# Kernel tuning notes

Measured on AMD Instinct MI355X. Metric: run time of the kernel, lower is better.

Reference implementation:

```python
import jax, jax.numpy as jnp
import numpy as np

SEQ, B, XD = 2048, 4, 16
D, NH, DFF, L, M = 256, 8, 512, 2, 1024
DH = D // NH
NEG_INF = -1e9  # finite stand-in for -inf (same softmax result, grad-safe)


def setup_inputs() -> dict:
    key = jax.random.key(0)
    ks = iter(jax.random.split(key, 40))

    def w(shape, s=0.02):
        return jax.random.normal(next(ks), shape, dtype=jnp.float32) * s

    return {
        "x": jax.random.normal(next(ks), (SEQ, B, XD), dtype=jnp.float32),
        "y": jax.random.normal(next(ks), (SEQ, B), dtype=jnp.float32),
        "single_eval_pos": M,
        "xenc_w": w((D, XD)), "xenc_b": w((D,)),
        "yenc_w": w((D, 1)), "yenc_b": w((D,)),
        "in_proj_w": w((L, 3 * D, D)), "in_proj_b": w((L, 3 * D)),
        "out_proj_w": w((L, D, D)), "out_proj_b": w((L, D)),
        "ln1_g": jnp.ones((L, D), jnp.float32), "ln1_b": jnp.zeros((L, D), jnp.float32),
        "lin1_w": w((L, DFF, D)), "lin1_b": w((L, DFF)),
        "lin2_w": w((L, D, DFF)), "lin2_b": w((L, D)),
        "ln2_g": jnp.ones((L, D), jnp.float32), "ln2_b": jnp.zeros((L, D), jnp.float32),
        "head_w1": w((DFF, D)), "head_b1": w((DFF,)),
        "head_w2": w((1, DFF)), "head_b2": w((1,)),
    }


def _layer_norm(x, g, b, eps=1e-5):
    mu = jnp.mean(x, axis=-1, keepdims=True)
    var = jnp.var(x, axis=-1, keepdims=True)
    return (x - mu) * jax.lax.rsqrt(var + eps) * g + b


def _forward(x, y, M_, p):
    seq, batch = y.shape
    x_src = x @ p["xenc_w"].T + p["xenc_b"]                     # [seq, b, D]
    y_src = y[..., None] @ p["yenc_w"].T + p["yenc_b"]           # [seq, b, D]
    tokens = jnp.concatenate([x_src[:M_] + y_src[:M_], x_src[M_:]], axis=0)

    # prefix-block + diagonal mask: keep (j < M) or (i == j)
    i = jnp.arange(seq)
    keep = (i[None, :] < M_) | (i[:, None] == i[None, :])
    mask = jnp.where(keep, 0.0, NEG_INF).astype(tokens.dtype)    # [seq, seq]

    h = tokens
    for l in range(p["in_proj_w"].shape[0]):
        qkv = h @ p["in_proj_w"][l].T + p["in_proj_b"][l]        # [seq, b, 3D]
        q, k, v = jnp.split(qkv, 3, axis=-1)
        to_heads = lambda t: t.reshape(seq, batch, NH, DH).transpose(1, 2, 0, 3)
        q, k, v = to_heads(q), to_heads(k), to_heads(v)          # [b, h, s, dh]
        scores = jnp.einsum("bhqd,bhkd->bhqk", q, k) / np.float32(np.sqrt(DH)) + mask
        attn = jax.nn.softmax(scores, axis=-1)
        o = jnp.einsum("bhqk,bhkd->bhqd", attn, v)
        o = o.transpose(2, 0, 1, 3).reshape(seq, batch, D)
        o = o @ p["out_proj_w"][l].T + p["out_proj_b"][l]
        h = _layer_norm(h + o, p["ln1_g"][l], p["ln1_b"][l])      # post-norm
        ff = jax.nn.gelu(h @ p["lin1_w"][l].T + p["lin1_b"][l], approximate=False)
        ff = ff @ p["lin2_w"][l].T + p["lin2_b"][l]
        h = _layer_norm(h + ff, p["ln2_g"][l], p["ln2_b"][l])

    q_out = h[M_:]                                               # [seq-M, b, D]
    hid = jax.nn.gelu(q_out @ p["head_w1"].T + p["head_b1"], approximate=False)
    return hid @ p["head_w2"].T + p["head_b2"]                   # [seq-M, b, 1]


def reference(x, y, single_eval_pos, xenc_w, xenc_b, yenc_w, yenc_b,
              in_proj_w, in_proj_b, out_proj_w, out_proj_b,
              ln1_g, ln1_b, lin1_w, lin1_b, lin2_w, lin2_b, ln2_g, ln2_b,
              head_w1, head_b1, head_w2, head_b2):
    p = dict(xenc_w=xenc_w, xenc_b=xenc_b, yenc_w=yenc_w, yenc_b=yenc_b,
             in_proj_w=in_proj_w, in_proj_b=in_proj_b,
             out_proj_w=out_proj_w, out_proj_b=out_proj_b,
             ln1_g=ln1_g, ln1_b=ln1_b, lin1_w=lin1_w, lin1_b=lin1_b,
             lin2_w=lin2_w, lin2_b=lin2_b, ln2_g=ln2_g, ln2_b=ln2_b,
             head_w1=head_w1, head_b1=head_b1, head_w2=head_w2, head_b2=head_b2)
    return _forward(x, y, int(single_eval_pos), p)
```

## Files before the change

### kernel.cpp

```cpp
#include <hip/hip_runtime.h>
#include <hip/hip_bf16.h>
#include <math.h>

#define SEQ    2048
#define BATCH  4
#define XDIM   16
#define DMODEL 256
#define NHEAD  8
#define DH     32
#define DFF    512
#define NLAYER 2
#define MPOS   1024
#define ROWS   (SEQ*BATCH)

#define ATT_SCALE 0.17677669529663687f
#define BK 32

typedef __attribute__((ext_vector_type(8))) short bf16x8;
typedef __attribute__((ext_vector_type(4))) float f32x4;

__device__ __forceinline__ float gelu_exact(float x) {
    return 0.5f * x * (1.0f + erff(x * 0.70710678118654752f));
}
__device__ __forceinline__ short f2bf(float f) {
    unsigned int u = __float_as_uint(f);
    u += 0x7FFFu + ((u >> 16) & 1u);
    return (short)(u >> 16);
}
__device__ __forceinline__ float bf2f(unsigned short u) {
    return __uint_as_float(((unsigned int)u) << 16);
}
__device__ __forceinline__ void gload16(const unsigned short* g, unsigned short* l) {
    __builtin_amdgcn_global_load_lds(
        (const __attribute__((address_space(1))) unsigned int*)g,
        (__attribute__((address_space(3))) unsigned int*)l, 16, 0, 0);
}
#define VMWAIT(N) asm volatile("s_waitcnt vmcnt(" #N ")" ::: "memory")
__device__ __forceinline__ void pipe_barrier() {
    __builtin_amdgcn_sched_barrier(0);
    __builtin_amdgcn_s_barrier();
    __builtin_amdgcn_sched_barrier(0);
}

__global__ __launch_bounds__(256) void encode_cast(
    const float* __restrict__ x, const float* __restrict__ y,
    const float* __restrict__ xw, const float* __restrict__ xb,
    const float* __restrict__ yw, const float* __restrict__ yb,
    float* __restrict__ h, unsigned short* __restrict__ hb,
    const float* __restrict__ s0, const float* __restrict__ s1,
    const float* __restrict__ s2, const float* __restrict__ s3,
    const float* __restrict__ s4,
    unsigned short* __restrict__ d0, unsigned short* __restrict__ d1,
    unsigned short* __restrict__ d2, unsigned short* __restrict__ d3,
    unsigned short* __restrict__ d4)
{
    if (blockIdx.x < ROWS) {
        int row = blockIdx.x;
        int d   = threadIdx.x;
        int s   = row / BATCH;
        __shared__ float xs[XDIM];
        __shared__ float ys;
        if (d < XDIM) xs[d] = x[(size_t)row*XDIM + d];
        if (d == 0)   ys    = y[row];
        __syncthreads();
        float acc = xb[d];
        #pragma unroll
        for (int k = 0; k < XDIM; ++k) acc = fmaf(xs[k], xw[d*XDIM + k], acc);
        if (s < MPOS) acc += ys * yw[d] + yb[d];
        h[(size_t)row*DMODEL + d]  = acc;
        hb[(size_t)row*DMODEL + d] = (unsigned short)f2bf(acc);
        return;
    }
    int i = (blockIdx.x - ROWS)*256 + threadIdx.x;
    if (i >= 147456) return;
    const float* s; unsigned short* d; int off;
    if      (i <  49152) { s = s0; d = d0; off = i; }
    else if (i <  65536) { s = s1; d = d1; off = i - 49152; }
    else if (i <  98304) { s = s2; d = d2; off = i - 65536; }
    else if (i < 131072) { s = s3; d = d3; off = i - 98304; }
    else                 { s = s4; d = d4; off = i - 131072; }
    float4 a = *(const float4*)(s + (size_t)off*8);
    float4 c = *(const float4*)(s + (size_t)off*8 + 4);
    ushort4 u0, u1;
    u0.x=(unsigned short)f2bf(a.x); u0.y=(unsigned short)f2bf(a.y);
    u0.z=(unsigned short)f2bf(a.z); u0.w=(unsigned short)f2bf(a.w);
    u1.x=(unsigned short)f2bf(c.x); u1.y=(unsigned short)f2bf(c.y);
    u1.z=(unsigned short)f2bf(c.z); u1.w=(unsigned short)f2bf(c.w);
    *(ushort4*)(d + (size_t)off*8)     = u0;
    *(ushort4*)(d + (size_t)off*8 + 4) = u1;
}

__global__ __launch_bounds__(256) void gemm_qkv(
    const unsigned short* __restrict__ A, const unsigned short* __restrict__ B,
    const float* __restrict__ bias,
    unsigned short* __restrict__ Qg, unsigned short* __restrict__ Kg,
    unsigned short* __restrict__ Vg, int K)
{
    __shared__ unsigned short As[3][128][BK];
    __shared__ unsigned short Bs[3][64][BK];
    int tid  = threadIdx.x;
    int w    = tid >> 6, lane = tid & 63;
    int col  = lane & 15, quad = lane >> 4;
    int m0   = blockIdx.y * 128, n0 = blockIdx.x * 64;
    int l4   = lane >> 2, c8 = (lane & 3) * 8;

    f32x4 acc[2][4];
    #pragma unroll
    for (int i = 0; i < 2; ++i)
        #pragma unroll
        for (int j = 0; j < 4; ++j) acc[i][j] = (f32x4){0.f,0.f,0.f,0.f};

    const unsigned short* ga = A + (size_t)(m0 + w*32 + l4)*K + c8;
    const unsigned short* gb = B + (size_t)(n0 + w*16 + l4)*K + c8;

    const int NS = K / BK;
    gload16(ga,                  &As[0][w*32     ][0]);
    gload16(ga + (size_t)16*K,   &As[0][w*32 + 16][0]);
    gload16(gb,                  &Bs[0][w*16     ][0]);
    gload16(ga + BK,                  &As[1][w*32     ][0]);
    gload16(ga + BK + (size_t)16*K,   &As[1][w*32 + 16][0]);
    gload16(gb + BK,                  &Bs[1][w*16     ][0]);

    int bcur = 0;
    for (int s = 0; s < NS; ++s) {
        if (s == NS - 1) { VMWAIT(0); } else { VMWAIT(3); }
        pipe_barrier();
        if (s + 2 < NS) {
            int bpre = bcur + 2; if (bpre >= 3) bpre -= 3;
            int k2 = (s + 2) * BK;
            gload16(ga + k2,                &As[bpre][w*32     ][0]);
            gload16(ga + k2 + (size_t)16*K, &As[bpre][w*32 + 16][0]);
            gload16(gb + k2,                &Bs[bpre][w*16     ][0]);
        }
        bf16x8 af[2], bfr[4];
        #pragma unroll
        for (int i = 0; i < 2; ++i) af[i]  = *(const bf16x8*)&As[bcur][w*32 + i*16 + col][quad*8];
        #pragma unroll
        for (int j = 0; j < 4; ++j) bfr[j] = *(const bf16x8*)&Bs[bcur][j*16 + col][quad*8];
        #pragma unroll
        for (int i = 0; i < 2; ++i)
            #pragma unroll
            for (int j = 0; j < 4; ++j)
                acc[i][j] = __builtin_amdgcn_mfma_f32_16x16x32_bf16(bfr[j], af[i], acc[i][j], 0, 0, 0);
        bcur = (bcur == 2) ? 0 : bcur + 1;
    }

    int region = n0 >> 8;
    if (region < 2) {
        #pragma unroll
        for (int i = 0; i < 2; ++i) {
            int m = m0 + w*32 + i*16 + col;
            int s = m >> 2, bidx = m & 3;
            #pragma unroll
            for (int j = 0; j < 4; ++j) {
                int ng = n0 + j*16 + quad*4;
                float4 bi = *(const float4*)&bias[ng];
                ushort4 u;
                u.x=(unsigned short)f2bf(acc[i][j][0] + bi.x);
                u.y=(unsigned short)f2bf(acc[i][j][1] + bi.y);
                u.z=(unsigned short)f2bf(acc[i][j][2] + bi.z);
                u.w=(unsigned short)f2bf(acc[i][j][3] + bi.w);
                int np = ng - (region << 8);
                int hh = np >> 5, d = np & 31;
                int bh = bidx*NHEAD + hh;
                if (region == 0)
                    *(ushort4*)(Qg + ((size_t)(bh*SEQ + s))*DH + d) = u;
                else
                    *(ushort4*)(Kg + ((size_t)(bh*SEQ + s))*DH + d) = u;
            }
        }
    } else {
        __syncthreads();
        unsigned short* T3 = (unsigned short*)As;
        #pragma unroll
        for (int i = 0; i < 2; ++i) {
            int mi = w*32 + i*16 + col;
            int ss = mi >> 2, bidx = mi & 3;
            #pragma unroll
            for (int j = 0; j < 4; ++j) {
                int ni = j*16 + quad*4;
                float4 bi = *(const float4*)&bias[n0 + ni];
                T3[((ni    )*4 + bidx)*32 + ss] = (unsigned short)f2bf(acc[i][j][0] + bi.x);
                T3[((ni + 1)*4 + bidx)*32 + ss] = (unsigned short)f2bf(acc[i][j][1] + bi.y);
                T3[((ni + 2)*4 + bidx)*32 + ss] = (unsigned short)f2bf(acc[i][j][2] + bi.z);
                T3[((ni + 3)*4 + bidx)*32 + ss] = (unsigned short)f2bf(acc[i][j][3] + bi.w);
            }
        }
        __syncthreads();
        int sBase = m0 >> 2;
        #pragma unroll
        for (int r = 0; r < 4; ++r) {
            int chunk = tid + 256*r;
            int l = chunk >> 2, p = chunk & 3;
            int d = l & 31, hh_l = (l >> 5) & 1, bidx = l >> 6;
            int ni = hh_l*32 + d;
            int hh = ((n0 & 255) + ni) >> 5;
            int bh = bidx*NHEAD + hh;
            uint4 val = *(const uint4*)&T3[(ni*4 + bidx)*32 + p*8];
            *(uint4*)(Vg + ((size_t)(bh*DH + d))*SEQ + sBase + p*8) = val;
        }
    }
}

__global__ __launch_bounds__(256) void attn_mfma(
    const unsigned short* __restrict__ Qg,
    const unsigned short* __restrict__ Kg,
    const unsigned short* __restrict__ Vg,
    unsigned short* __restrict__ o)
{
    const int id = blockIdx.x;
    const int sl = id >> 3;
    const int bh = (id & 7) * 4 + (sl >> 5);
    const int qt = sl & 31;
    const int h  = bh & 7;
    const int b  = bh >> 3;
    const int q0 = qt * 64;
    const int tid  = threadIdx.x;
    const int w    = tid >> 6;
    const int lane = tid & 63;
    const int col  = lane & 15;
    const int quad = lane >> 4;

    __shared__ unsigned short Kt[2][64][40];
    __shared__ unsigned short Vt[2][32][72];
    __shared__ unsigned short Pt[4][16][72];

    const int q = q0 + 16*w + col;
    bf16x8 qf = *(const bf16x8*)(Qg + ((size_t)(bh*SEQ + q))*DH + quad*8);

    f32x4 O0 = {0.f,0.f,0.f,0.f};
    f32x4 O1 = {0.f,0.f,0.f,0.f};
    float lsum = 0.f;

    const int kRow = tid >> 2, kCh = (tid & 3) * 8;
    const int vD   = tid >> 3, vCh = (tid & 7) * 8;

    const int nT = 16 + ((q0 >= MPOS) ? 1 : 0);
    uint4 kreg = *(const uint4*)(Kg + ((size_t)(bh*SEQ + kRow))*DH + kCh);
    uint4 vreg = *(const uint4*)(Vg + ((size_t)(bh*DH + vD))*SEQ + vCh);

    for (int kt = 0; kt < nT; ++kt) {
        const bool self = (kt == 16);
        const int  p    = kt & 1;
        *(uint4*)&Kt[p][kRow][kCh] = kreg;
        *(uint4*)&Vt[p][vD][vCh]   = vreg;
        __syncthreads();
        if (kt + 1 < nT) {
            int kn = (kt + 1 == 16) ? q0 : (kt + 1)*64;
            kreg = *(const uint4*)(Kg + ((size_t)(bh*SEQ + kn + kRow))*DH + kCh);
            vreg = *(const uint4*)(Vg + ((size_t)(bh*DH + vD))*SEQ + kn + vCh);
        }

        #pragma unroll
        for (int mt = 0; mt < 4; ++mt) {
            bf16x8 kf = *(const bf16x8*)&Kt[p][mt*16 + col][quad*8];
            f32x4 st = {0.f,0.f,0.f,0.f};
            st = __builtin_amdgcn_mfma_f32_16x16x32_bf16(kf, qf, st, 0, 0, 0);
            ushort4 pw;
            #pragma unroll
            for (int i = 0; i < 4; ++i) {
                float pv = __expf(st[i]*ATT_SCALE);
                if (self && (mt*16 + quad*4 + i != 16*w + col)) pv = 0.f;
                unsigned short us = (unsigned short)f2bf(pv);
                ((unsigned short*)&pw)[i] = us;
                lsum += bf2f(us);
            }
            *(ushort4*)&Pt[w][col][mt*16 + quad*4] = pw;
        }
        #pragma unroll
        for (int c = 0; c < 2; ++c) {
            bf16x8 pf = *(const bf16x8*)&Pt[w][col][c*32 + quad*8];
            bf16x8 v0 = *(const bf16x8*)&Vt[p][col     ][c*32 + quad*8];
            bf16x8 v1 = *(const bf16x8*)&Vt[p][col + 16][c*32 + quad*8];
            O0 = __builtin_amdgcn_mfma_f32_16x16x32_bf16(v0, pf, O0, 0, 0, 0);
            O1 = __builtin_amdgcn_mfma_f32_16x16x32_bf16(v1, pf, O1, 0, 0, 0);
        }
    }

    lsum += __shfl_xor(lsum, 16, 64);
    lsum += __shfl_xor(lsum, 32, 64);
    float inv = 1.0f / lsum;
    ushort4 u0, u1;
    #pragma unroll
    for (int i = 0; i < 4; ++i) {
        ((unsigned short*)&u0)[i] = (unsigned short)f2bf(O0[i]*inv);
        ((unsigned short*)&u1)[i] = (unsigned short)f2bf(O1[i]*inv);
    }
    unsigned short* op = o + ((size_t)(q*BATCH + b))*DMODEL + h*DH;
    *(ushort4*)(op + quad*4)      = u0;
    *(ushort4*)(op + 16 + quad*4) = u1;
}

__global__ __launch_bounds__(256, 2) void mlp_fused(
    const unsigned short* __restrict__ attb,
    const unsigned short* __restrict__ Wout, const float* __restrict__ ob,
    const float* __restrict__ g1, const float* __restrict__ be1,
    const unsigned short* __restrict__ W1, const float* __restrict__ fb1,
    const unsigned short* __restrict__ W2, const float* __restrict__ fb2,
    const float* __restrict__ g2, const float* __restrict__ be2,
    float* __restrict__ h, unsigned short* __restrict__ hb,
    const unsigned short* __restrict__ Wh1, const float* __restrict__ hb1,
    const float* __restrict__ hw2, const float* __restrict__ hb2,
    float* __restrict__ out, int doHead)
{
    __shared__ unsigned short Bs[3][256][BK];
    __shared__ unsigned short As[3][16][BK];
    __shared__ unsigned short Ht[16][264];
    __shared__ unsigned short Pt[16][520];
    __shared__ float sP[4][16], qP[4][16];

    const int tid  = threadIdx.x;
    const int w    = tid >> 6;
    const int lane = tid & 63;
    const int col  = lane & 15;
    const int quad = lane >> 4;
    const int l4   = lane >> 2;
    const int c8   = (lane & 3) * 8;
    const int bid  = blockIdx.x;
    const int m0   = ((bid >> 1) * 16) + ((bid & 1) * 4096);
    const int m    = m0 + col;

    float resid[4][4];

    {
        f32x4 acc[4];
        #pragma unroll
        for (int j = 0; j < 4; ++j) acc[j] = (f32x4){0.f,0.f,0.f,0.f};

        const unsigned short* ga = attb + (size_t)(m0 + l4)*DMODEL + c8;
        const unsigned short* gb = Wout + (size_t)(w*64 + l4)*DMODEL + c8;
        const int NS = DMODEL / BK;

        #pragma unroll
        for (int pb = 0; pb < 2; ++pb) {
            int k = pb * BK;
            if (w == 0) gload16(ga + k, &As[pb][0][0]);
            #pragma unroll
            for (int rr = 0; rr < 4; ++rr)
                gload16(gb + k + (size_t)(rr*16)*DMODEL, &Bs[pb][w*64 + rr*16][0]);
        }
        int bcur = 0;
        for (int s = 0; s < NS; ++s) {
            if (s == NS - 1)  { VMWAIT(0); }
            else if (w == 0)  { VMWAIT(5); }
            else              { VMWAIT(4); }
            pipe_barrier();
            if (s + 2 < NS) {
                int bpre = bcur + 2; if (bpre >= 3) bpre -= 3;
                int k2 = (s + 2) * BK;
                if (w == 0) gload16(ga + k2, &As[bpre][0][0]);
                #pragma unroll
                for (int rr = 0; rr < 4; ++rr)
                    gload16(gb + k2 + (size_t)(rr*16)*DMODEL, &Bs[bpre][w*64 + rr*16][0]);
            }
            bf16x8 af = *(const bf16x8*)&As[bcur][col][quad*8];
            #pragma unroll
            for (int j = 0; j < 4; ++j) {
                bf16x8 bfr = *(const bf16x8*)&Bs[bcur][w*64 + j*16 + col][quad*8];
                acc[j] = __builtin_amdgcn_mfma_f32_16x16x32_bf16(bfr, af, acc[j], 0, 0, 0);
            }
            bcur = (bcur == 2) ? 0 : bcur + 1;
        }

        float s = 0.f, q = 0.f;
        #pragma unroll
        for (int j = 0; j < 4; ++j) {
            int n = w*64 + j*16 + quad*4;
            float4 bi = *(const float4*)&ob[n];
            float4 hv = *(const float4*)&h[(size_t)m*DMODEL + n];
            #pragma unroll
            for (int i = 0; i < 4; ++i) {
                float val = acc[j][i] + ((const float*)&bi)[i] + ((const float*)&hv)[i];
                resid[j][i] = val;
                s += val; q += val*val;
            }
        }
        s += __shfl_xor(s, 16, 64); s += __shfl_xor(s, 32, 64);
        q += __shfl_xor(q, 16, 64); q += __shfl_xor(q, 32, 64);
        if (quad == 0) { sP[w][col] = s; qP[w][col] = q; }
        __syncthreads();
        float st = sP[0][col] + sP[1][col] + sP[2][col] + sP[3][col];
        float qt = qP[0][col] + qP[1][col] + qP[2][col] + qP[3][col];
        float mu   = st * (1.0f/DMODEL);
        float var  = qt * (1.0f/DMODEL) - mu*mu;
        float rstd = rsqrtf(var + 1e-5f);
        #pragma unroll
        for (int j = 0; j < 4; ++j) {
            int n = w*64 + j*16 + quad*4;
            float4 gv = *(const float4*)&g1[n];
            float4 bv = *(const float4*)&be1[n];
            ushort4 u;
            #pragma unroll
            for (int i = 0; i < 4; ++i) {
                float o = (resid[j][i]-mu)*rstd*((const float*)&gv)[i] + ((const float*)&bv)[i];
                resid[j][i] = o;
                ((unsigned short*)&u)[i] = (unsigned short)f2bf(o);
            }
            *(ushort4*)&Ht[col][n] = u;
        }
        __syncthreads();
    }

    #pragma unroll 1
    for (int nh = 0; nh < 2; ++nh) {
        f32x4 acc[4];
        #pragma unroll
        for (int j = 0; j < 4; ++j) acc[j] = (f32x4){0.f,0.f,0.f,0.f};
        const unsigned short* gb = W1 + (size_t)(nh*256 + w*64 + l4)*DMODEL + c8;
        const int NS = DMODEL / BK;

        #pragma unroll
        for (int pb = 0; pb < 2; ++pb)
            #pragma unroll
            for (int rr = 0; rr < 4; ++rr)
                gload16(gb + pb*BK + (size_t)(rr*16)*DMODEL, &Bs[pb][w*64 + rr*16][0]);

        int bcur = 0;
        for (int s = 0; s < NS; ++s) {
            if (s == NS - 1) { VMWAIT(0); } else { VMWAIT(4); }
            pipe_barrier();
            if (s + 2 < NS) {
                int bpre = bcur + 2; if (bpre >= 3) bpre -= 3;
                int k2 = (s + 2) * BK;
                #pragma unroll
                for (int rr = 0; rr < 4; ++rr)
                    gload16(gb + k2 + (size_t)(rr*16)*DMODEL, &Bs[bpre][w*64 + rr*16][0]);
            }
            bf16x8 af = *(const bf16x8*)&Ht[col][s*BK + quad*8];
            #pragma unroll
            for (int j = 0; j < 4; ++j) {
                bf16x8 bfr = *(const bf16x8*)&Bs[bcur][w*64 + j*16 + col][quad*8];
                acc[j] = __builtin_amdgcn_mfma_f32_16x16x32_bf16(bfr, af, acc[j], 0, 0, 0);
            }
            bcur = (bcur == 2) ? 0 : bcur + 1;
        }
        #pragma unroll
        for (int j = 0; j < 4; ++j) {
            int n2 = nh*256 + w*64 + j*16 + quad*4;
            float4 bi = *(const float4*)&fb1[n2];
            ushort4 u;
            #pragma unroll
            for (int i = 0; i < 4; ++i)
                ((unsigned short*)&u)[i] = (unsigned short)f2bf(gelu_exact(acc[j][i] + ((const float*)&bi)[i]));
            *(ushort4*)&Pt[col][n2] = u;
        }
        pipe_barrier();
    }

    {
        __syncthreads();
        f32x4 acc[4];
        #pragma unroll
        for (int j = 0; j < 4; ++j) acc[j] = (f32x4){0.f,0.f,0.f,0.f};
        const unsigned short* gb = W2 + (size_t)(w*64 + l4)*DFF + c8;
        const int NS = DFF / BK;

        #pragma unroll
        for (int pb = 0; pb < 2; ++pb)
            #pragma unroll
            for (int rr = 0; rr < 4; ++rr)
                gload16(gb + pb*BK + (size_t)(rr*16)*DFF, &Bs[pb][w*64 + rr*16][0]);

        int bcur = 0;
        for (int s = 0; s < NS; ++s) {
            if (s == NS - 1) { VMWAIT(0); } else { VMWAIT(4); }
            pipe_barrier();
            if (s + 2 < NS) {
                int bpre = bcur + 2; if (bpre >= 3) bpre -= 3;
                int k2 = (s + 2) * BK;
                #pragma unroll
                for (int rr = 0; rr < 4; ++rr)
                    gload16(gb + k2 + (size_t)(rr*16)*DFF, &Bs[bpre][w*64 + rr*16][0]);
            }
            bf16x8 af = *(const bf16x8*)&Pt[col][s*BK + quad*8];
            #pragma unroll
            for (int j = 0; j < 4; ++j) {
                bf16x8 bfr = *(const bf16x8*)&Bs[bcur][w*64 + j*16 + col][quad*8];
                acc[j] = __builtin_amdgcn_mfma_f32_16x16x32_bf16(bfr, af, acc[j], 0, 0, 0);
            }
            bcur = (bcur == 2) ? 0 : bcur + 1;
        }

        float s = 0.f, q = 0.f;
        float v[4][4];
        #pragma unroll
        for (int j = 0; j < 4; ++j) {
            int n = w*64 + j*16 + quad*4;
            float4 bi = *(const float4*)&fb2[n];
            #pragma unroll
            for (int i = 0; i < 4; ++i) {
                float val = acc[j][i] + ((const float*)&bi)[i] + resid[j][i];
                v[j][i] = val;
                s += val; q += val*val;
            }
        }
        s += __shfl_xor(s, 16, 64); s += __shfl_xor(s, 32, 64);
        q += __shfl_xor(q, 16, 64); q += __shfl_xor(q, 32, 64);
        if (quad == 0) { sP[w][col] = s; qP[w][col] = q; }
        __syncthreads();
        float st = sP[0][col] + sP[1][col] + sP[2][col] + sP[3][col];
        float qt = qP[0][col] + qP[1][col] + qP[2][col] + qP[3][col];
        float mu   = st * (1.0f/DMODEL);
        float var  = qt * (1.0f/DMODEL) - mu*mu;
        float rstd = rsqrtf(var + 1e-5f);
        #pragma unroll
        for (int j = 0; j < 4; ++j) {
            int n = w*64 + j*16 + quad*4;
            float4 gv = *(const float4*)&g2[n];
            float4 bv = *(const float4*)&be2[n];
            float4 o;
            ushort4 u;
            #pragma unroll
            for (int i = 0; i < 4; ++i) {
                float ov = (v[j][i]-mu)*rstd*((const float*)&gv)[i] + ((const float*)&bv)[i];
                ((float*)&o)[i] = ov;
                ((unsigned short*)&u)[i] = (unsigned short)f2bf(ov);
            }
            *(float4*)&h[(size_t)m*DMODEL + n] = o;
            *(ushort4*)(hb + (size_t)m*DMODEL + n) = u;
            *(ushort4*)&Ht[col][n] = u;
        }
        __syncthreads();
    }

    if (doHead && m0 >= 4096) {
        float sdot = 0.f;
        #pragma unroll 1
        for (int nh = 0; nh < 2; ++nh) {
            f32x4 acc[4];
            #pragma unroll
            for (int j = 0; j < 4; ++j) acc[j] = (f32x4){0.f,0.f,0.f,0.f};
            const unsigned short* gb = Wh1 + (size_t)(nh*256 + w*64 + l4)*DMODEL + c8;
            const int NS = DMODEL / BK;

            #pragma unroll
            for (int pb = 0; pb < 2; ++pb)
                #pragma unroll
                for (int rr = 0; rr < 4; ++rr)
                    gload16(gb + pb*BK + (size_t)(rr*16)*DMODEL, &Bs[pb][w*64 + rr*16][0]);

            int bcur = 0;
            for (int s = 0; s < NS; ++s) {
                if (s == NS - 1) { VMWAIT(0); } else { VMWAIT(4); }
                pipe_barrier();
                if (s + 2 < NS) {
                    int bpre = bcur + 2; if (bpre >= 3) bpre -= 3;
                    int k2 = (s + 2) * BK;
                    #pragma unroll
                    for (int rr = 0; rr < 4; ++rr)
                        gload16(gb + k2 + (size_t)(rr*16)*DMODEL, &Bs[bpre][w*64 + rr*16][0]);
                }
                bf16x8 af = *(const bf16x8*)&Ht[col][s*BK + quad*8];
                #pragma unroll
                for (int j = 0; j < 4; ++j) {
                    bf16x8 bfr = *(const bf16x8*)&Bs[bcur][w*64 + j*16 + col][quad*8];
                    acc[j] = __builtin_amdgcn_mfma_f32_16x16x32_bf16(bfr, af, acc[j], 0, 0, 0);
                }
                bcur = (bcur == 2) ? 0 : bcur + 1;
            }
            #pragma unroll
            for (int j = 0; j < 4; ++j) {
                int n2 = nh*256 + w*64 + j*16 + quad*4;
                float4 b1v = *(const float4*)&hb1[n2];
                float4 w2v = *(const float4*)&hw2[n2];
                #pragma unroll
                for (int i = 0; i < 4; ++i)
                    sdot += gelu_exact(acc[j][i] + ((const float*)&b1v)[i]) * ((const float*)&w2v)[i];
            }
            pipe_barrier();
        }
        sdot += __shfl_xor(sdot, 16, 64); sdot += __shfl_xor(sdot, 32, 64);
        if (quad == 0) sP[w][col] = sdot;
        __syncthreads();
        if (tid < 16)
            out[(m0 - 4096) + tid] = sP[0][tid] + sP[1][tid] + sP[2][tid] + sP[3][tid] + hb2[0];
    }
}

extern "C" void kernel_launch(void* const* d_in, const int* in_sizes, int n_in,
                              void* d_out, int out_size, void* d_ws, size_t ws_size,
                              hipStream_t stream)
{
    const float* x        = (const float*)d_in[0];
    const float* y        = (const float*)d_in[1];
    const float* xenc_w   = (const float*)d_in[3];
    const float* xenc_b   = (const float*)d_in[4];
    const float* yenc_w   = (const float*)d_in[5];
    const float* yenc_b   = (const float*)d_in[6];
    const float* in_proj_w  = (const float*)d_in[7];
    const float* in_proj_b  = (const float*)d_in[8];
    const float* out_proj_w = (const float*)d_in[9];
    const float* out_proj_b = (const float*)d_in[10];
    const float* ln1_g    = (const float*)d_in[11];
    const float* ln1_b    = (const float*)d_in[12];
    const float* lin1_w   = (const float*)d_in[13];
    const float* lin1_b   = (const float*)d_in[14];
    const float* lin2_w   = (const float*)d_in[15];
    const float* lin2_b   = (const float*)d_in[16];
    const float* ln2_g    = (const float*)d_in[17];
    const float* ln2_b    = (const float*)d_in[18];
    const float* head_w1  = (const float*)d_in[19];
    const float* head_b1  = (const float*)d_in[20];
    const float* head_w2  = (const float*)d_in[21];
    const float* head_b2  = (const float*)d_in[22];
    float* out = (float*)d_out;

    float* ws  = (float*)d_ws;
    float* h    = ws;
    unsigned short* hb    = (unsigned short*)(h + (size_t)ROWS*DMODEL);
    unsigned short* attb  = hb    + (size_t)ROWS*DMODEL;
    unsigned short* Qg    = attb  + (size_t)ROWS*DMODEL;
    unsigned short* Kg    = Qg    + (size_t)BATCH*NHEAD*SEQ*DH;
    unsigned short* Vg    = Kg    + (size_t)BATCH*NHEAD*SEQ*DH;
    unsigned short* Wqkv  = Vg    + (size_t)BATCH*NHEAD*SEQ*DH;
    unsigned short* Wout  = Wqkv  + (size_t)NLAYER*3*DMODEL*DMODEL;
    unsigned short* Wl1   = Wout  + (size_t)NLAYER*DMODEL*DMODEL;
    unsigned short* Wl2   = Wl1   + (size_t)NLAYER*DFF*DMODEL;
    unsigned short* Wh1   = Wl2   + (size_t)NLAYER*DMODEL*DFF;

    encode_cast<<<ROWS + 576, 256, 0, stream>>>(
        x, y, xenc_w, xenc_b, yenc_w, yenc_b, h, hb,
        in_proj_w, out_proj_w, lin1_w, lin2_w, head_w1,
        Wqkv, Wout, Wl1, Wl2, Wh1);

    for (int l = 0; l < NLAYER; ++l) {
        gemm_qkv<<<dim3(12, ROWS/128), 256, 0, stream>>>(
            hb, Wqkv + (size_t)l*3*DMODEL*DMODEL, in_proj_b + l*3*DMODEL,
            Qg, Kg, Vg, DMODEL);
        attn_mfma<<<dim3(SEQ/64 * NHEAD * BATCH), 256, 0, stream>>>(Qg, Kg, Vg, attb);
        mlp_fused<<<ROWS/16, 256, 0, stream>>>(
            attb,
            Wout + (size_t)l*DMODEL*DMODEL, out_proj_b + l*DMODEL,
            ln1_g + l*DMODEL, ln1_b + l*DMODEL,
            Wl1 + (size_t)l*DFF*DMODEL, lin1_b + l*DFF,
            Wl2 + (size_t)l*DMODEL*DFF, lin2_b + l*DMODEL,
            ln2_g + l*DMODEL, ln2_b + l*DMODEL,
            h, hb,
            Wh1, head_b1, head_w2, head_b2,
            out, (l == NLAYER-1) ? 1 : 0);
    }
}
```

Baseline: 260.1 us.

## Process two 16-row groups per block in fused MLP to reuse weight tiles

Each mlp_fused block now handles two 16-row tiles, one from the context half and one from the query half, and shares every loaded weight tile across both with paired MFMAs. The grid shrinks from 512 to 256 blocks, which halves weight traffic into LDS per row. The head path now runs in every block on the query-half tile. The cost is double the accumulator registers and LDS per block, with the two-blocks-per-CU launch bound removed and fewer blocks available to fill the CUs.

```diff
diff --git a/kernel.cpp b/kernel.cpp
--- a/kernel.cpp
+++ b/kernel.cpp
@@ -291,7 +291,7 @@
     *(ushort4*)(op + 16 + quad*4) = u1;
 }
 
-__global__ __launch_bounds__(256, 2) void mlp_fused(
+__global__ __launch_bounds__(256) void mlp_fused(
     const unsigned short* __restrict__ attb,
     const unsigned short* __restrict__ Wout, const float* __restrict__ ob,
     const float* __restrict__ g1, const float* __restrict__ be1,
@@ -304,10 +304,10 @@
     float* __restrict__ out, int doHead)
 {
     __shared__ unsigned short Bs[3][256][BK];
-    __shared__ unsigned short As[3][16][BK];
-    __shared__ unsigned short Ht[16][264];
-    __shared__ unsigned short Pt[16][520];
-    __shared__ float sP[4][16], qP[4][16];
+    __shared__ unsigned short As[3][2][16][BK];
+    __shared__ unsigned short Ht[2][16][264];
+    __shared__ unsigned short Pt[2][16][520];
+    __shared__ float sP[2][4][16], qP[2][4][16];
 
     const int tid  = threadIdx.x;
     const int w    = tid >> 6;
@@ -317,24 +317,32 @@
     const int l4   = lane >> 2;
     const int c8   = (lane & 3) * 8;
     const int bid  = blockIdx.x;
-    const int m0   = ((bid >> 1) * 16) + ((bid & 1) * 4096);
-    const int m    = m0 + col;
-
-    float resid[4][4];
+    const int m0a  = bid * 16;
+    const int m0b  = 4096 + bid * 16;
+    const int ma   = m0a + col;
+    const int mb   = m0b + col;
+
+    float resid[2][4][4];
 
     {
-        f32x4 acc[4];
-        #pragma unroll
-        for (int j = 0; j < 4; ++j) acc[j] = (f32x4){0.f,0.f,0.f,0.f};
-
-        const unsigned short* ga = attb + (size_t)(m0 + l4)*DMODEL + c8;
-        const unsigned short* gb = Wout + (size_t)(w*64 + l4)*DMODEL + c8;
+        f32x4 acc[2][4];
+        #pragma unroll
+        for (int g = 0; g < 2; ++g)
+            #pragma unroll
+            for (int j = 0; j < 4; ++j) acc[g][j] = (f32x4){0.f,0.f,0.f,0.f};
+
+        const unsigned short* ga0 = attb + (size_t)(m0a + l4)*DMODEL + c8;
+        const unsigned short* ga1 = attb + (size_t)(m0b + l4)*DMODEL + c8;
+        const unsigned short* gb  = Wout + (size_t)(w*64 + l4)*DMODEL + c8;
         const int NS = DMODEL / BK;
 
         #pragma unroll
         for (int pb = 0; pb < 2; ++pb) {
             int k = pb * BK;
-            if (w == 0) gload16(ga + k, &As[pb][0][0]);
+            if (w == 0) {
+                gload16(ga0 + k, &As[pb][0][0][0]);
+                gload16(ga1 + k, &As[pb][1][0][0]);
+            }
             #pragma unroll
             for (int rr = 0; rr < 4; ++rr)
                 gload16(gb + k + (size_t)(rr*16)*DMODEL, &Bs[pb][w*64 + rr*16][0]);
@@ -342,70 +350,90 @@
         int bcur = 0;
         for (int s = 0; s < NS; ++s) {
             if (s == NS - 1)  { VMWAIT(0); }
-            else if (w == 0)  { VMWAIT(5); }
+            else if (w == 0)  { VMWAIT(6); }
             else              { VMWAIT(4); }
             pipe_barrier();
             if (s + 2 < NS) {
                 int bpre = bcur + 2; if (bpre >= 3) bpre -= 3;
                 int k2 = (s + 2) * BK;
-                if (w == 0) gload16(ga + k2, &As[bpre][0][0]);
+                if (w == 0) {
+                    gload16(ga0 + k2, &As[bpre][0][0][0]);
+                    gload16(ga1 + k2, &As[bpre][1][0][0]);
+                }
                 #pragma unroll
                 for (int rr = 0; rr < 4; ++rr)
                     gload16(gb + k2 + (size_t)(rr*16)*DMODEL, &Bs[bpre][w*64 + rr*16][0]);
             }
-            bf16x8 af = *(const bf16x8*)&As[bcur][col][quad*8];
+            bf16x8 af0 = *(const bf16x8*)&As[bcur][0][col][quad*8];
+            bf16x8 af1 = *(const bf16x8*)&As[bcur][1][col][quad*8];
             #pragma unroll
             for (int j = 0; j < 4; ++j) {
                 bf16x8 bfr = *(const bf16x8*)&Bs[bcur][w*64 + j*16 + col][quad*8];
-                acc[j] = __builtin_amdgcn_mfma_f32_16x16x32_bf16(bfr, af, acc[j], 0, 0, 0);
+                acc[0][j] = __builtin_amdgcn_mfma_f32_16x16x32_bf16(bfr, af0, acc[0][j], 0, 0, 0);
+                acc[1][j] = __builtin_amdgcn_mfma_f32_16x16x32_bf16(bfr, af1, acc[1][j], 0, 0, 0);
             }
             bcur = (bcur == 2) ? 0 : bcur + 1;
         }
 
-        float s = 0.f, q = 0.f;
-        #pragma unroll
-        for (int j = 0; j < 4; ++j) {
-            int n = w*64 + j*16 + quad*4;
-            float4 bi = *(const float4*)&ob[n];
-            float4 hv = *(const float4*)&h[(size_t)m*DMODEL + n];
-            #pragma unroll
-            for (int i = 0; i < 4; ++i) {
-                float val = acc[j][i] + ((const float*)&bi)[i] + ((const float*)&hv)[i];
-                resid[j][i] = val;
-                s += val; q += val*val;
-            }
-        }
-        s += __shfl_xor(s, 16, 64); s += __shfl_xor(s, 32, 64);
-        q += __shfl_xor(q, 16, 64); q += __shfl_xor(q, 32, 64);
-        if (quad == 0) { sP[w][col] = s; qP[w][col] = q; }
-        __syncthreads();
-        float st = sP[0][col] + sP[1][col] + sP[2][col] + sP[3][col];
-        float qt = qP[0][col] + qP[1][col] + qP[2][col] + qP[3][col];
-        float mu   = st * (1.0f/DMODEL);
-        float var  = qt * (1.0f/DMODEL) - mu*mu;
-        float rstd = rsqrtf(var + 1e-5f);
-        #pragma unroll
-        for (int j = 0; j < 4; ++j) {
-            int n = w*64 + j*16 + quad*4;
-            float4 gv = *(const float4*)&g1[n];
-            float4 bv = *(const float4*)&be1[n];
-            ushort4 u;
-            #pragma unroll
-            for (int i = 0; i < 4; ++i) {
-                float o = (resid[j][i]-mu)*rstd*((const float*)&gv)[i] + ((const float*)&bv)[i];
-                resid[j][i] = o;
-                ((unsigned short*)&u)[i] = (unsigned short)f2bf(o);
-            }
-            *(ushort4*)&Ht[col][n] = u;
+        float ssum[2] = {0.f, 0.f}, qsum[2] = {0.f, 0.f};
+        #pragma unroll
+        for (int g = 0; g < 2; ++g) {
+            int m = g ? mb : ma;
+            #pragma unroll
+            for (int j = 0; j < 4; ++j) {
+                int n = w*64 + j*16 + quad*4;
+                float4 bi = *(const float4*)&ob[n];
+                float4 hv = *(const float4*)&h[(size_t)m*DMODEL + n];
+                #pragma unroll
+                for (int i = 0; i < 4; ++i) {
+                    float val = acc[g][j][i] + ((const float*)&bi)[i] + ((const float*)&hv)[i];
+                    resid[g][j][i] = val;
+                    ssum[g] += val; qsum[g] += val*val;
+                }
+            }
+        }
+        #pragma unroll
+        for (int g = 0; g < 2; ++g) {
+            ssum[g] += __shfl_xor(ssum[g], 16, 64); ssum[g] += __shfl_xor(ssum[g], 32, 64);
+            qsum[g] += __shfl_xor(qsum[g], 16, 64); qsum[g] += __shfl_xor(qsum[g], 32, 64);
+        }
+        if (quad == 0) {
+            sP[0][w][col] = ssum[0]; qP[0][w][col] = qsum[0];
+            sP[1][w][col] = ssum[1]; qP[1][w][col] = qsum[1];
+        }
+        __syncthreads();
+        #pragma unroll
+        for (int g = 0; g < 2; ++g) {
+            float st = sP[g][0][col] + sP[g][1][col] + sP[g][2][col] + sP[g][3][col];
+            float qt = qP[g][0][col] + qP[g][1][col] + qP[g][2][col] + qP[g][3][col];
+            float mu   = st * (1.0f/DMODEL);
+            float var  = qt * (1.0f/DMODEL) - mu*mu;
+            float rstd = rsqrtf(var + 1e-5f);
+            #pragma unroll
+            for (int j = 0; j < 4; ++j) {
+                int n = w*64 + j*16 + quad*4;
+                float4 gv = *(const float4*)&g1[n];
+                float4 bv = *(const float4*)&be1[n];
+                ushort4 u;
+                #pragma unroll
+                for (int i = 0; i < 4; ++i) {
+                    float o = (resid[g][j][i]-mu)*rstd*((const float*)&gv)[i] + ((const float*)&bv)[i];
+                    resid[g][j][i] = o;
+                    ((unsigned short*)&u)[i] = (unsigned short)f2bf(o);
+                }
+                *(ushort4*)&Ht[g][col][n] = u;
+            }
         }
         __syncthreads();
     }
 
     #pragma unroll 1
     for (int nh = 0; nh < 2; ++nh) {
-        f32x4 acc[4];
-        #pragma unroll
-        for (int j = 0; j < 4; ++j) acc[j] = (f32x4){0.f,0.f,0.f,0.f};
+        f32x4 acc[2][4];
+        #pragma unroll
+        for (int g = 0; g < 2; ++g)
+            #pragma unroll
+            for (int j = 0; j < 4; ++j) acc[g][j] = (f32x4){0.f,0.f,0.f,0.f};
         const unsigned short* gb = W1 + (size_t)(nh*256 + w*64 + l4)*DMODEL + c8;
         const int NS = DMODEL / BK;
 
@@ -426,32 +454,38 @@
                 for (int rr = 0; rr < 4; ++rr)
                     gload16(gb + k2 + (size_t)(rr*16)*DMODEL, &Bs[bpre][w*64 + rr*16][0]);
             }
-            bf16x8 af = *(const bf16x8*)&Ht[col][s*BK + quad*8];
+            bf16x8 af0 = *(const bf16x8*)&Ht[0][col][s*BK + quad*8];
+            bf16x8 af1 = *(const bf16x8*)&Ht[1][col][s*BK + quad*8];
             #pragma unroll
             for (int j = 0; j < 4; ++j) {
                 bf16x8 bfr = *(const bf16x8*)&Bs[bcur][w*64 + j*16 + col][quad*8];
-                acc[j] = __builtin_amdgcn_mfma_f32_16x16x32_bf16(bfr, af, acc[j], 0, 0, 0);
+                acc[0][j] = __builtin_amdgcn_mfma_f32_16x16x32_bf16(bfr, af0, acc[0][j], 0, 0, 0);
+                acc[1][j] = __builtin_amdgcn_mfma_f32_16x16x32_bf16(bfr, af1, acc[1][j], 0, 0, 0);
             }
             bcur = (bcur == 2) ? 0 : bcur + 1;
         }
         #pragma unroll
-        for (int j = 0; j < 4; ++j) {
-            int n2 = nh*256 + w*64 + j*16 + quad*4;
-            float4 bi = *(const float4*)&fb1[n2];
-            ushort4 u;
-            #pragma unroll
-            for (int i = 0; i < 4; ++i)
-                ((unsigned short*)&u)[i] = (unsigned short)f2bf(gelu_exact(acc[j][i] + ((const float*)&bi)[i]));
-            *(ushort4*)&Pt[col][n2] = u;
-        }
+        for (int g = 0; g < 2; ++g)
+            #pragma unroll
+            for (int j = 0; j < 4; ++j) {
+                int n2 = nh*256 + w*64 + j*16 + quad*4;
+                float4 bi = *(const float4*)&fb1[n2];
+                ushort4 u;
+                #pragma unroll
+                for (int i = 0; i < 4; ++i)
+                    ((unsigned short*)&u)[i] = (unsigned short)f2bf(gelu_exact(acc[g][j][i] + ((const float*)&bi)[i]));
+                *(ushort4*)&Pt[g][col][n2] = u;
+            }
         pipe_barrier();
     }
 
     {
         __syncthreads();
-        f32x4 acc[4];
-        #pragma unroll
-        for (int j = 0; j < 4; ++j) acc[j] = (f32x4){0.f,0.f,0.f,0.f};
+        f32x4 acc[2][4];
+        #pragma unroll
+        for (int g = 0; g < 2; ++g)
+            #pragma unroll
+            for (int j = 0; j < 4; ++j) acc[g][j] = (f32x4){0.f,0.f,0.f,0.f};
         const unsigned short* gb = W2 + (size_t)(w*64 + l4)*DFF + c8;
         const int NS = DFF / BK;
 
@@ -472,58 +506,71 @@
                 for (int rr = 0; rr < 4; ++rr)
                     gload16(gb + k2 + (size_t)(rr*16)*DFF, &Bs[bpre][w*64 + rr*16][0]);
             }
-            bf16x8 af = *(const bf16x8*)&Pt[col][s*BK + quad*8];
+            bf16x8 af0 = *(const bf16x8*)&Pt[0][col][s*BK + quad*8];
+            bf16x8 af1 = *(const bf16x8*)&Pt[1][col][s*BK + quad*8];
             #pragma unroll
             for (int j = 0; j < 4; ++j) {
                 bf16x8 bfr = *(const bf16x8*)&Bs[bcur][w*64 + j*16 + col][quad*8];
-                acc[j] = __builtin_amdgcn_mfma_f32_16x16x32_bf16(bfr, af, acc[j], 0, 0, 0);
+                acc[0][j] = __builtin_amdgcn_mfma_f32_16x16x32_bf16(bfr, af0, acc[0][j], 0, 0, 0);
+                acc[1][j] = __builtin_amdgcn_mfma_f32_16x16x32_bf16(bfr, af1, acc[1][j], 0, 0, 0);
             }
             bcur = (bcur == 2) ? 0 : bcur + 1;
         }
 
-        float s = 0.f, q = 0.f;
-        float v[4][4];
-        #pragma unroll
-        for (int j = 0; j < 4; ++j) {
-            int n = w*64 + j*16 + quad*4;
-            float4 bi = *(const float4*)&fb2[n];
-            #pragma unroll
-            for (int i = 0; i < 4; ++i) {
-                float val = acc[j][i] + ((const float*)&bi)[i] + resid[j][i];
-                v[j][i] = val;
-                s += val; q += val*val;
-            }
-        }
-        s += __shfl_xor(s, 16, 64); s += __shfl_xor(s, 32, 64);
-        q += __shfl_xor(q, 16, 64); q += __shfl_xor(q, 32, 64);
-        if (quad == 0) { sP[w][col] = s; qP[w][col] = q; }
-        __syncthreads();
-        float st = sP[0][col] + sP[1][col] + sP[2][col] + sP[3][col];
-        float qt = qP[0][col] + qP[1][col] + qP[2][col] + qP[3][col];
-        float mu   = st * (1.0f/DMODEL);
-        float var  = qt * (1.0f/DMODEL) - mu*mu;
-        float rstd = rsqrtf(var + 1e-5f);
-        #pragma unroll
-        for (int j = 0; j < 4; ++j) {
-            int n = w*64 + j*16 + quad*4;
-            float4 gv = *(const float4*)&g2[n];
-            float4 bv = *(const float4*)&be2[n];
-            float4 o;
-            ushort4 u;
-            #pragma unroll
-            for (int i = 0; i < 4; ++i) {
-                float ov = (v[j][i]-mu)*rstd*((const float*)&gv)[i] + ((const float*)&bv)[i];
-                ((float*)&o)[i] = ov;
-                ((unsigned short*)&u)[i] = (unsigned short)f2bf(ov);
-            }
-            *(float4*)&h[(size_t)m*DMODEL + n] = o;
-            *(ushort4*)(hb + (size_t)m*DMODEL + n) = u;
-            *(ushort4*)&Ht[col][n] = u;
-        }
-        __syncthreads();
-    }
-
-    if (doHead && m0 >= 4096) {
+        float ssum[2] = {0.f, 0.f}, qsum[2] = {0.f, 0.f};
+        #pragma unroll
+        for (int g = 0; g < 2; ++g)
+            #pragma unroll
+            for (int j = 0; j < 4; ++j) {
+                int n = w*64 + j*16 + quad*4;
+                float4 bi = *(const float4*)&fb2[n];
+                #pragma unroll
+                for (int i = 0; i < 4; ++i) {
+                    float val = acc[g][j][i] + ((const float*)&bi)[i] + resid[g][j][i];
+                    resid[g][j][i] = val;
+                    ssum[g] += val; qsum[g] += val*val;
+                }
+            }
+        #pragma unroll
+        for (int g = 0; g < 2; ++g) {
+            ssum[g] += __shfl_xor(ssum[g], 16, 64); ssum[g] += __shfl_xor(ssum[g], 32, 64);
+            qsum[g] += __shfl_xor(qsum[g], 16, 64); qsum[g] += __shfl_xor(qsum[g], 32, 64);
+        }
+        if (quad == 0) {
+            sP[0][w][col] = ssum[0]; qP[0][w][col] = qsum[0];
+            sP[1][w][col] = ssum[1]; qP[1][w][col] = qsum[1];
+        }
+        __syncthreads();
+        #pragma unroll
+        for (int g = 0; g < 2; ++g) {
+            int m = g ? mb : ma;
+            float st = sP[g][0][col] + sP[g][1][col] + sP[g][2][col] + sP[g][3][col];
+            float qt = qP[g][0][col] + qP[g][1][col] + qP[g][2][col] + qP[g][3][col];
+            float mu   = st * (1.0f/DMODEL);
+            float var  = qt * (1.0f/DMODEL) - mu*mu;
+            float rstd = rsqrtf(var + 1e-5f);
+            #pragma unroll
+            for (int j = 0; j < 4; ++j) {
+                int n = w*64 + j*16 + quad*4;
+                float4 gv = *(const float4*)&g2[n];
+                float4 bv = *(const float4*)&be2[n];
+                float4 o;
+                ushort4 u;
+                #pragma unroll
+                for (int i = 0; i < 4; ++i) {
+                    float ov = (resid[g][j][i]-mu)*rstd*((const float*)&gv)[i] + ((const float*)&bv)[i];
+                    ((float*)&o)[i] = ov;
+                    ((unsigned short*)&u)[i] = (unsigned short)f2bf(ov);
+                }
+                *(float4*)&h[(size_t)m*DMODEL + n] = o;
+                *(ushort4*)(hb + (size_t)m*DMODEL + n) = u;
+                *(ushort4*)&Ht[g][col][n] = u;
+            }
+        }
+        __syncthreads();
+    }
+
+    if (doHead) {
         float sdot = 0.f;
         #pragma unroll 1
         for (int nh = 0; nh < 2; ++nh) {
@@ -550,7 +597,7 @@
                     for (int rr = 0; rr < 4; ++rr)
                         gload16(gb + k2 + (size_t)(rr*16)*DMODEL, &Bs[bpre][w*64 + rr*16][0]);
                 }
-                bf16x8 af = *(const bf16x8*)&Ht[col][s*BK + quad*8];
+                bf16x8 af = *(const bf16x8*)&Ht[1][col][s*BK + quad*8];
                 #pragma unroll
                 for (int j = 0; j < 4; ++j) {
                     bf16x8 bfr = *(const bf16x8*)&Bs[bcur][w*64 + j*16 + col][quad*8];
@@ -570,10 +617,10 @@
             pipe_barrier();
         }
         sdot += __shfl_xor(sdot, 16, 64); sdot += __shfl_xor(sdot, 32, 64);
-        if (quad == 0) sP[w][col] = sdot;
+        if (quad == 0) sP[0][w][col] = sdot;
         __syncthreads();
         if (tid < 16)
-            out[(m0 - 4096) + tid] = sP[0][tid] + sP[1][tid] + sP[2][tid] + sP[3][tid] + hb2[0];
+            out[bid*16 + tid] = sP[0][0][tid] + sP[0][1][tid] + sP[0][2][tid] + sP[0][3][tid] + hb2[0];
     }
 }
 
@@ -628,7 +675,7 @@
             hb, Wqkv + (size_t)l*3*DMODEL*DMODEL, in_proj_b + l*3*DMODEL,
             Qg, Kg, Vg, DMODEL);
         attn_mfma<<<dim3(SEQ/64 * NHEAD * BATCH), 256, 0, stream>>>(Qg, Kg, Vg, attb);
-        mlp_fused<<<ROWS/16, 256, 0, stream>>>(
+        mlp_fused<<<256, 256, 0, stream>>>(
             attb,
             Wout + (size_t)l*DMODEL*DMODEL, out_proj_b + l*DMODEL,
             ln1_g + l*DMODEL, ln1_b + l*DMODEL,
```

New measurement: 258.4 us. Within noise of the previous version (-0.6%).
